# Optimization experiments

Hardware: AMD Instinct MI355X
Metric: run time of the kernel (lower is better)

## Reference

```python
import jax, jax.numpy as jnp
import numpy as np

B, L, D, DEG = 32, 1024, 512, 8
E = B * L * DEG  # 262144 edges total
N = B * L


def setup_inputs() -> dict:
    key = jax.random.key(0)
    ks = jax.random.split(key, 8)
    text_feature = jax.random.normal(ks[0], (B, L, D), jnp.float32)
    # edge list per sample (torch.nonzero(edge_matrix[i]) equivalent), offset by b*L like PyG batching
    src_local = jax.random.randint(ks[1], (E,), 0, L, jnp.int32)
    dst_local = jax.random.randint(ks[2], (E,), 0, L, jnp.int32)
    boff = (jnp.arange(E, dtype=jnp.int32) // (E // B)) * L
    edge_src = src_local + boff
    edge_dst = dst_local + boff
    s = 1.0 / np.sqrt(D)
    W1 = jax.random.uniform(ks[3], (D, D), jnp.float32, -s, s)   # node Linear
    b1 = jax.random.uniform(ks[4], (D,), jnp.float32, -s, s)
    gamma = jnp.ones((D,), jnp.float32)      # BatchNorm1d weight
    beta = jnp.zeros((D,), jnp.float32)      # BatchNorm1d bias
    run_mean = jnp.zeros((D,), jnp.float32)  # BN running stats (eval mode)
    run_var = jnp.ones((D,), jnp.float32)
    alpha1 = jnp.array(0.25, jnp.float32)    # PReLU (node MLP)
    Wg = jax.random.uniform(ks[5], (D, D), jnp.float32, -s, s)   # GCNConv lin (bias=False)
    bg = jnp.zeros((D,), jnp.float32)        # GCNConv bias
    alpha2 = jnp.array(0.25, jnp.float32)    # PReLU (after GCN)
    return {"text_feature": text_feature, "edge_src": edge_src, "edge_dst": edge_dst,
            "W1": W1, "b1": b1, "gamma": gamma, "beta": beta,
            "run_mean": run_mean, "run_var": run_var, "alpha1": alpha1,
            "Wg": Wg, "bg": bg, "alpha2": alpha2}


def reference(text_feature, edge_src, edge_dst, W1, b1, gamma, beta,
              run_mean, run_var, alpha1, Wg, bg, alpha2):
    Bs, Ls, Ds = text_feature.shape
    Nn = Bs * Ls
    xf = text_feature.reshape(Nn, Ds)
    # node MLP: Linear -> BatchNorm1d (eval) -> PReLU
    h = xf @ W1 + b1
    h = (h - run_mean) * jax.lax.rsqrt(run_var + 1e-5) * gamma + beta
    h = jnp.where(h >= 0, h, alpha1 * h)
    # GCNConv: add self loops, symmetric degree norm, gather->scatter-add, + bias
    nodes = jnp.arange(Nn, dtype=edge_src.dtype)
    src = jnp.concatenate([edge_src, nodes])
    dst = jnp.concatenate([edge_dst, nodes])
    deg = jnp.zeros((Nn,), h.dtype).at[dst].add(1.0)  # in-degree incl. self loop, >= 1
    dinv = jax.lax.rsqrt(deg)
    xw = h @ Wg                               # [N, D]
    msg = (xw * dinv[:, None])[src]           # gather D^{-1/2}-scaled messages [E+N, D]
    agg = jnp.zeros_like(xw).at[dst].add(msg) * dinv[:, None]
    g = agg + bg
    g = jnp.where(g >= 0, g, alpha2 * g)      # PReLU
    g = g.reshape(Bs, Ls, Ds)
    # F.normalize(p=2, dim=2) + residual (original input)
    g = g / jnp.clip(jnp.linalg.norm(g, axis=2, keepdims=True), 1e-12)
    return g + text_feature
```

## Files before the change

### kernel.cpp

```cpp
#include <hip/hip_runtime.h>
#include <math.h>

#define DD    512
#define NN    32768
#define EE    262144

typedef float f32x4 __attribute__((ext_vector_type(4)));
typedef __bf16 bf16x8 __attribute__((ext_vector_type(8)));
typedef __bf16 bf16x4 __attribute__((ext_vector_type(4)));

__global__ void k_zero(int* __restrict__ cnt) {
    int i = blockIdx.x * 256 + threadIdx.x;
    if (i < NN) cnt[i] = 0;
}

__global__ void k_count(const int* __restrict__ dst, int* __restrict__ cnt) {
    int e = blockIdx.x * 256 + threadIdx.x;
    if (e < EE) atomicAdd(&cnt[dst[e]], 1);
}

__global__ __launch_bounds__(1024) void k_scan(
    const int* __restrict__ cnt, int* __restrict__ offs,
    int* __restrict__ cursor, float* __restrict__ dinv)
{
    __shared__ int part[1024];
    int t = threadIdx.x;
    int base = t * 32;
    int local[32];
    int s = 0;
#pragma unroll
    for (int i = 0; i < 32; ++i) { local[i] = s; s += cnt[base + i]; }
    part[t] = s;
    __syncthreads();
    for (int off = 1; off < 1024; off <<= 1) {
        int v = (t >= off) ? part[t - off] : 0;
        __syncthreads();
        part[t] += v;
        __syncthreads();
    }
    int prev = (t == 0) ? 0 : part[t - 1];
#pragma unroll
    for (int i = 0; i < 32; ++i) {
        int o = prev + local[i];
        offs[base + i] = o;
        cursor[base + i] = o;
        dinv[base + i] = rsqrtf((float)cnt[base + i] + 1.0f);
    }
    if (t == 1023) offs[NN] = part[1023];
}

__global__ void k_fill(const int* __restrict__ src, const int* __restrict__ dst,
                       int* __restrict__ cursor, int* __restrict__ csr) {
    int e = blockIdx.x * 256 + threadIdx.x;
    if (e < EE) {
        int d = dst[e];
        int p = atomicAdd(&cursor[d], 1);
        csr[p] = src[e];
    }
}

__global__ __launch_bounds__(256) void k_wt(const float* __restrict__ W1, const float* __restrict__ Wg,
                                            __bf16* __restrict__ W1t, __bf16* __restrict__ Wgt) {
    __shared__ float tile[32][33];
    const float* W = blockIdx.z ? Wg : W1;
    __bf16* Wt = blockIdx.z ? Wgt : W1t;
    int x0 = blockIdx.x * 32;
    int y0 = blockIdx.y * 32;
    int tx = threadIdx.x;
    for (int j = threadIdx.y; j < 32; j += 8)
        tile[j][tx] = W[(size_t)(y0 + j) * DD + x0 + tx];
    __syncthreads();
    for (int j = threadIdx.y; j < 32; j += 8)
        Wt[(size_t)(x0 + j) * DD + y0 + tx] = (__bf16)tile[tx][j];
}

template <int MODE>
__global__ __launch_bounds__(256) void k_gemm_mfma(
    const void* __restrict__ Ap,
    const __bf16* __restrict__ Bt,
    __bf16* __restrict__ Cout,
    const float* __restrict__ bias,
    const float* __restrict__ gamma, const float* __restrict__ beta,
    const float* __restrict__ mean, const float* __restrict__ var,
    const float* __restrict__ alphap,
    const float* __restrict__ dinv)
{
    __shared__ __bf16 lds[2][128 * 32];

    const int tid  = threadIdx.x;
    const int lane = tid & 63;
    const int w    = tid >> 6;
    const int wm   = (w >> 1) * 64;
    const int wn   = (w & 1) * 64;
    const int work = ((blockIdx.x & 7) << 7) + (blockIdx.x >> 3);
    const int m0   = (work >> 2) * 128;
    const int n0   = (work & 3) * 128;

    f32x4 acc[4][4] = {};

    for (int k0 = 0; k0 < DD; k0 += 32) {
        __syncthreads();
#pragma unroll
        for (int rd = 0; rd < 2; ++rd) {
            int cbase = rd * 256 + w * 64;
            int cidx = cbase + lane;
            int r = cidx >> 2, s = cidx & 3;
            int c = s ^ ((r >> 1) & 3);
            const __bf16* gb = Bt + (size_t)(n0 + r) * DD + k0 + c * 8;
            __builtin_amdgcn_global_load_lds(
                (const __attribute__((address_space(1))) unsigned int*)gb,
                (__attribute__((address_space(3))) unsigned int*)(&lds[1][cbase * 8]), 16, 0, 0);
        }
        if constexpr (MODE == 1) {
            const float* A = (const float*)Ap;
#pragma unroll
            for (int hh = 0; hh < 2; ++hh) {
                int ci = tid + hh * 256;
                int r = ci >> 2, s = ci & 3;
                int c = s ^ ((r >> 1) & 3);
                const float* ga = A + (size_t)(m0 + r) * DD + k0 + c * 8;
                float4 f0 = *(const float4*)ga;
                float4 f1 = *(const float4*)(ga + 4);
                bf16x8 o;
                o[0] = (__bf16)f0.x; o[1] = (__bf16)f0.y; o[2] = (__bf16)f0.z; o[3] = (__bf16)f0.w;
                o[4] = (__bf16)f1.x; o[5] = (__bf16)f1.y; o[6] = (__bf16)f1.z; o[7] = (__bf16)f1.w;
                *(bf16x8*)&lds[0][ci * 8] = o;
            }
        } else {
            const __bf16* A = (const __bf16*)Ap;
#pragma unroll
            for (int rd = 0; rd < 2; ++rd) {
                int cbase = rd * 256 + w * 64;
                int cidx = cbase + lane;
                int r = cidx >> 2, s = cidx & 3;
                int c = s ^ ((r >> 1) & 3);
                const __bf16* ga = A + (size_t)(m0 + r) * DD + k0 + c * 8;
                __builtin_amdgcn_global_load_lds(
                    (const __attribute__((address_space(1))) unsigned int*)ga,
                    (__attribute__((address_space(3))) unsigned int*)(&lds[0][cbase * 8]), 16, 0, 0);
            }
        }
        __syncthreads();

        bf16x8 af[4], bf[4];
#pragma unroll
        for (int m = 0; m < 4; ++m) {
            int r = wm + m * 16 + (lane & 15);
            int s = (lane >> 4) ^ ((r >> 1) & 3);
            af[m] = *(const bf16x8*)&lds[0][r * 32 + s * 8];
            int q = wn + m * 16 + (lane & 15);
            int sq = (lane >> 4) ^ ((q >> 1) & 3);
            bf[m] = *(const bf16x8*)&lds[1][q * 32 + sq * 8];
        }
#pragma unroll
        for (int m = 0; m < 4; ++m)
#pragma unroll
            for (int n = 0; n < 4; ++n)
                acc[m][n] = __builtin_amdgcn_mfma_f32_16x16x32_bf16(af[m], bf[n], acc[m][n], 0, 0, 0);
    }

    float alpha = (MODE == 1) ? alphap[0] : 0.0f;
#pragma unroll
    for (int m = 0; m < 4; ++m) {
        int row_base = m0 + wm + m * 16 + ((lane >> 4) << 2);
#pragma unroll
        for (int n = 0; n < 4; ++n) {
            int col = n0 + wn + n * 16 + (lane & 15);
#pragma unroll
            for (int j = 0; j < 4; ++j) {
                int row = row_base + j;
                float x = acc[m][n][j];
                if (MODE == 1) {
                    x += bias[col];
                    x = (x - mean[col]) * rsqrtf(var[col] + 1e-5f) * gamma[col] + beta[col];
                    x = (x >= 0.0f) ? x : alpha * x;
                } else {
                    x *= dinv[row];
                }
                Cout[(size_t)row * DD + col] = (__bf16)x;
            }
        }
    }
}

__global__ __launch_bounds__(256) void k_gather_final(
    const int* __restrict__ offs, const int* __restrict__ csr,
    const __bf16* __restrict__ xws, const float* __restrict__ dinv,
    const float* __restrict__ bg, const float* __restrict__ alpha2,
    const float* __restrict__ text, float* __restrict__ out)
{
    int blk = blockIdx.x;
    int sb  = ((blk & 7) << 10) + (blk >> 3);
    int wave = threadIdx.x >> 6;
    int lane = threadIdx.x & 63;
    int node = sb * 4 + wave;
    int c = lane * 8;
    int beg = offs[node], end = offs[node + 1];
    int ne = end - beg;

    bf16x8 sv = *(const bf16x8*)(xws + (size_t)node * DD + c);
    float a[8];
#pragma unroll
    for (int i = 0; i < 8; ++i) a[i] = (float)sv[i];

    int k = 0;
    for (; k + 4 <= ne; k += 4) {
        int s0 = csr[beg + k + 0];
        int s1 = csr[beg + k + 1];
        int s2 = csr[beg + k + 2];
        int s3 = csr[beg + k + 3];
        bf16x8 v0 = *(const bf16x8*)(xws + (size_t)s0 * DD + c);
        bf16x8 v1 = *(const bf16x8*)(xws + (size_t)s1 * DD + c);
        bf16x8 v2 = *(const bf16x8*)(xws + (size_t)s2 * DD + c);
        bf16x8 v3 = *(const bf16x8*)(xws + (size_t)s3 * DD + c);
#pragma unroll
        for (int i = 0; i < 8; ++i)
            a[i] += (float)v0[i] + (float)v1[i] + (float)v2[i] + (float)v3[i];
    }
    for (; k < ne; ++k) {
        int s = csr[beg + k];
        bf16x8 v = *(const bf16x8*)(xws + (size_t)s * DD + c);
#pragma unroll
        for (int i = 0; i < 8; ++i) a[i] += (float)v[i];
    }

    float di = dinv[node];
    float al = alpha2[0];
    float g[8];
    float ss = 0.0f;
#pragma unroll
    for (int i = 0; i < 8; ++i) {
        float x = a[i] * di + bg[c + i];
        x = (x >= 0.0f) ? x : al * x;
        g[i] = x;
        ss += x * x;
    }
#pragma unroll
    for (int off = 1; off < 64; off <<= 1) ss += __shfl_xor(ss, off, 64);
    float inv = 1.0f / fmaxf(sqrtf(ss), 1e-12f);

    float4 t0 = *(const float4*)(text + (size_t)node * DD + c);
    float4 t1 = *(const float4*)(text + (size_t)node * DD + c + 4);
    float4 o0, o1;
    o0.x = g[0] * inv + t0.x; o0.y = g[1] * inv + t0.y;
    o0.z = g[2] * inv + t0.z; o0.w = g[3] * inv + t0.w;
    o1.x = g[4] * inv + t1.x; o1.y = g[5] * inv + t1.y;
    o1.z = g[6] * inv + t1.z; o1.w = g[7] * inv + t1.w;
    *(float4*)(out + (size_t)node * DD + c)     = o0;
    *(float4*)(out + (size_t)node * DD + c + 4) = o1;
}

extern "C" void kernel_launch(void* const* d_in, const int* in_sizes, int n_in,
                              void* d_out, int out_size, void* d_ws, size_t ws_size,
                              hipStream_t stream) {
    const float* text   = (const float*)d_in[0];
    const int*   esrc   = (const int*)d_in[1];
    const int*   edst   = (const int*)d_in[2];
    const float* W1     = (const float*)d_in[3];
    const float* b1     = (const float*)d_in[4];
    const float* gamma  = (const float*)d_in[5];
    const float* beta   = (const float*)d_in[6];
    const float* rmean  = (const float*)d_in[7];
    const float* rvar   = (const float*)d_in[8];
    const float* alpha1 = (const float*)d_in[9];
    const float* Wg     = (const float*)d_in[10];
    const float* bg     = (const float*)d_in[11];
    const float* alpha2 = (const float*)d_in[12];
    float* out = (float*)d_out;

    char* p = (char*)d_ws;
    auto alloc = [&](size_t bytes) { char* r = p; p += (bytes + 255) & ~(size_t)255; return r; };
    int*    cnt     = (int*)alloc((size_t)NN * 4);
    int*    offs    = (int*)alloc((size_t)(NN + 1) * 4);
    int*    cursor  = (int*)alloc((size_t)NN * 4);
    float*  dinv    = (float*)alloc((size_t)NN * 4);
    int*    csr     = (int*)alloc((size_t)EE * 4);
    __bf16* W1t     = (__bf16*)alloc((size_t)DD * DD * 2);
    __bf16* Wgt     = (__bf16*)alloc((size_t)DD * DD * 2);
    __bf16* h_bf    = (__bf16*)alloc((size_t)NN * DD * 2);
    __bf16* xws     = (__bf16*)alloc((size_t)NN * DD * 2);

    k_zero<<<NN / 256, 256, 0, stream>>>(cnt);
    k_count<<<EE / 256, 256, 0, stream>>>(edst, cnt);
    k_scan<<<1, 1024, 0, stream>>>(cnt, offs, cursor, dinv);
    k_fill<<<EE / 256, 256, 0, stream>>>(esrc, edst, cursor, csr);

    k_wt<<<dim3(16, 16, 2), dim3(32, 8), 0, stream>>>(W1, Wg, W1t, Wgt);

    k_gemm_mfma<1><<<1024, 256, 0, stream>>>(text, W1t, h_bf, b1, gamma, beta, rmean, rvar, alpha1, nullptr);

    k_gemm_mfma<2><<<1024, 256, 0, stream>>>(h_bf, Wgt, xws, nullptr, nullptr, nullptr, nullptr, nullptr, nullptr, dinv);

    k_gather_final<<<NN / 4, 256, 0, stream>>>(offs, csr, xws, dinv, bg, alpha2, text, out);
}
```

Before: 154.4 us.

## Double-buffer GEMM LDS tiles to overlap global loads with MFMA compute

Splits the shared-memory tile into separate double-buffered A and B buffers and software-pipelines the K loop. The next K-slice is prefetched (via global_load_lds, or into registers for the fp32 A path) while the current slice feeds the MFMAs. This leaves one barrier per iteration instead of two. It is meant to hide global-load latency behind matrix math, at the cost of doubled LDS use and extra registers, which may lower occupancy.

```diff
diff --git a/kernel.cpp b/kernel.cpp
--- a/kernel.cpp
+++ b/kernel.cpp
@@ -85,7 +85,8 @@
     const float* __restrict__ alphap,
     const float* __restrict__ dinv)
 {
-    __shared__ __bf16 lds[2][128 * 32];
+    __shared__ __bf16 As[2][128 * 32];
+    __shared__ __bf16 Bs[2][128 * 32];
 
     const int tid  = threadIdx.x;
     const int lane = tid & 63;
@@ -97,9 +98,9 @@
     const int n0   = (work & 3) * 128;
 
     f32x4 acc[4][4] = {};
-
-    for (int k0 = 0; k0 < DD; k0 += 32) {
-        __syncthreads();
+    float4 fa[2][2];
+
+    auto stageB = [&](int bb, int k0) {
 #pragma unroll
         for (int rd = 0; rd < 2; ++rd) {
             int cbase = rd * 256 + w * 64;
@@ -109,54 +110,92 @@
             const __bf16* gb = Bt + (size_t)(n0 + r) * DD + k0 + c * 8;
             __builtin_amdgcn_global_load_lds(
                 (const __attribute__((address_space(1))) unsigned int*)gb,
-                (__attribute__((address_space(3))) unsigned int*)(&lds[1][cbase * 8]), 16, 0, 0);
-        }
-        if constexpr (MODE == 1) {
-            const float* A = (const float*)Ap;
-#pragma unroll
-            for (int hh = 0; hh < 2; ++hh) {
-                int ci = tid + hh * 256;
-                int r = ci >> 2, s = ci & 3;
-                int c = s ^ ((r >> 1) & 3);
-                const float* ga = A + (size_t)(m0 + r) * DD + k0 + c * 8;
-                float4 f0 = *(const float4*)ga;
-                float4 f1 = *(const float4*)(ga + 4);
-                bf16x8 o;
-                o[0] = (__bf16)f0.x; o[1] = (__bf16)f0.y; o[2] = (__bf16)f0.z; o[3] = (__bf16)f0.w;
-                o[4] = (__bf16)f1.x; o[5] = (__bf16)f1.y; o[6] = (__bf16)f1.z; o[7] = (__bf16)f1.w;
-                *(bf16x8*)&lds[0][ci * 8] = o;
-            }
-        } else {
-            const __bf16* A = (const __bf16*)Ap;
-#pragma unroll
-            for (int rd = 0; rd < 2; ++rd) {
-                int cbase = rd * 256 + w * 64;
-                int cidx = cbase + lane;
-                int r = cidx >> 2, s = cidx & 3;
-                int c = s ^ ((r >> 1) & 3);
-                const __bf16* ga = A + (size_t)(m0 + r) * DD + k0 + c * 8;
-                __builtin_amdgcn_global_load_lds(
-                    (const __attribute__((address_space(1))) unsigned int*)ga,
-                    (__attribute__((address_space(3))) unsigned int*)(&lds[0][cbase * 8]), 16, 0, 0);
-            }
-        }
-        __syncthreads();
-
-        bf16x8 af[4], bf[4];
+                (__attribute__((address_space(3))) unsigned int*)(&Bs[bb][cbase * 8]), 16, 0, 0);
+        }
+    };
+    auto stageA_lds = [&](int bb, int k0) {
+        const __bf16* A = (const __bf16*)Ap;
+#pragma unroll
+        for (int rd = 0; rd < 2; ++rd) {
+            int cbase = rd * 256 + w * 64;
+            int cidx = cbase + lane;
+            int r = cidx >> 2, s = cidx & 3;
+            int c = s ^ ((r >> 1) & 3);
+            const __bf16* ga = A + (size_t)(m0 + r) * DD + k0 + c * 8;
+            __builtin_amdgcn_global_load_lds(
+                (const __attribute__((address_space(1))) unsigned int*)ga,
+                (__attribute__((address_space(3))) unsigned int*)(&As[bb][cbase * 8]), 16, 0, 0);
+        }
+    };
+    auto loadA = [&](int k0) {
+        const float* A = (const float*)Ap;
+#pragma unroll
+        for (int hh = 0; hh < 2; ++hh) {
+            int ci = tid + hh * 256;
+            int r = ci >> 2, s = ci & 3;
+            int c = s ^ ((r >> 1) & 3);
+            const float* ga = A + (size_t)(m0 + r) * DD + k0 + c * 8;
+            fa[hh][0] = *(const float4*)ga;
+            fa[hh][1] = *(const float4*)(ga + 4);
+        }
+    };
+    auto writeA = [&](int bb) {
+#pragma unroll
+        for (int hh = 0; hh < 2; ++hh) {
+            int ci = tid + hh * 256;
+            bf16x8 o;
+            o[0] = (__bf16)fa[hh][0].x; o[1] = (__bf16)fa[hh][0].y;
+            o[2] = (__bf16)fa[hh][0].z; o[3] = (__bf16)fa[hh][0].w;
+            o[4] = (__bf16)fa[hh][1].x; o[5] = (__bf16)fa[hh][1].y;
+            o[6] = (__bf16)fa[hh][1].z; o[7] = (__bf16)fa[hh][1].w;
+            *(bf16x8*)&As[bb][ci * 8] = o;
+        }
+    };
+
+    if constexpr (MODE == 1) {
+        loadA(0);
+        stageB(0, 0);
+        writeA(0);
+    } else {
+        stageA_lds(0, 0);
+        stageB(0, 0);
+    }
+    __syncthreads();
+
+#pragma unroll
+    for (int kt = 0; kt < 16; ++kt) {
+        const int cur = kt & 1;
+        const int nxt = cur ^ 1;
+        const int k1  = (kt + 1) * 32;
+
+        bf16x8 af[4], bfr[4];
 #pragma unroll
         for (int m = 0; m < 4; ++m) {
             int r = wm + m * 16 + (lane & 15);
             int s = (lane >> 4) ^ ((r >> 1) & 3);
-            af[m] = *(const bf16x8*)&lds[0][r * 32 + s * 8];
+            af[m] = *(const bf16x8*)&As[cur][r * 32 + s * 8];
             int q = wn + m * 16 + (lane & 15);
             int sq = (lane >> 4) ^ ((q >> 1) & 3);
-            bf[m] = *(const bf16x8*)&lds[1][q * 32 + sq * 8];
-        }
+            bfr[m] = *(const bf16x8*)&Bs[cur][q * 32 + sq * 8];
+        }
+
+        if (kt < 15) {
+            if constexpr (MODE == 1) loadA(k1);
+            else                     stageA_lds(nxt, k1);
+            stageB(nxt, k1);
+        }
+
 #pragma unroll
         for (int m = 0; m < 4; ++m)
 #pragma unroll
             for (int n = 0; n < 4; ++n)
-                acc[m][n] = __builtin_amdgcn_mfma_f32_16x16x32_bf16(af[m], bf[n], acc[m][n], 0, 0, 0);
+                acc[m][n] = __builtin_amdgcn_mfma_f32_16x16x32_bf16(af[m], bfr[n], acc[m][n], 0, 0, 0);
+
+        if constexpr (MODE == 1) {
+            if (kt < 15) writeA(nxt);
+        }
+
+        __syncthreads();
     }
 
     float alpha = (MODE == 1) ? alphap[0] : 0.0f;
```

After: 152.2 us. About the same (-1.4%).

## Keep weight slice in registers and stream A row slabs through LDS

Applied to the files above, without the earlier changes.

Replaces the 128x128 LDS-tiled GEMM with a weight-stationary kernel. Each wave holds a 32-column slice of the transposed weight (full K) in registers, and the block streams 32-row slabs of A (full K=512) through double-buffered LDS, so weight tiles are no longer reloaded for every K step. The BatchNorm affine transform is folded into a per-column scale and shift. The per-row dinv scaling moves from the second GEMM epilogue into the gather, which now applies dinv of each source node as it reads it. The change adds heavy register pressure (32 bf16x8 weight fragments per lane), only 256 blocks of 512 threads, small 32x32-per-wave MFMA tiles, and extra scalar dinv loads per edge.

```diff
diff --git a/kernel.cpp b/kernel.cpp
--- a/kernel.cpp
+++ b/kernel.cpp
@@ -7,7 +7,9 @@
 
 typedef float f32x4 __attribute__((ext_vector_type(4)));
 typedef __bf16 bf16x8 __attribute__((ext_vector_type(8)));
-typedef __bf16 bf16x4 __attribute__((ext_vector_type(4)));
+
+#define AS1 __attribute__((address_space(1)))
+#define AS3 __attribute__((address_space(3)))
 
 __global__ void k_zero(int* __restrict__ cnt) {
     int i = blockIdx.x * 256 + threadIdx.x;
@@ -75,111 +77,135 @@
 }
 
 template <int MODE>
-__global__ __launch_bounds__(256) void k_gemm_mfma(
+__global__ __launch_bounds__(512, 2) void k_gemm_w(
     const void* __restrict__ Ap,
-    const __bf16* __restrict__ Bt,
+    const __bf16* __restrict__ Wt,
     __bf16* __restrict__ Cout,
     const float* __restrict__ bias,
     const float* __restrict__ gamma, const float* __restrict__ beta,
     const float* __restrict__ mean, const float* __restrict__ var,
-    const float* __restrict__ alphap,
-    const float* __restrict__ dinv)
+    const float* __restrict__ alphap)
 {
-    __shared__ __bf16 lds[2][128 * 32];
-
-    const int tid  = threadIdx.x;
-    const int lane = tid & 63;
-    const int w    = tid >> 6;
-    const int wm   = (w >> 1) * 64;
-    const int wn   = (w & 1) * 64;
-    const int work = ((blockIdx.x & 7) << 7) + (blockIdx.x >> 3);
-    const int m0   = (work >> 2) * 128;
-    const int n0   = (work & 3) * 128;
-
-    f32x4 acc[4][4] = {};
-
-    for (int k0 = 0; k0 < DD; k0 += 32) {
+    __shared__ __bf16 slab[2][32 * DD];
+
+    const int t    = threadIdx.x;
+    const int lane = t & 63;
+    const int wv   = t >> 6;
+    const int work = ((blockIdx.x & 7) << 5) + (blockIdx.x >> 3);
+    const int nsl  = work & 1;
+    const int mb   = work >> 1;
+    const int mbase   = mb * 256;
+    const int colbase = nsl * 256 + wv * 32;
+
+    bf16x8 wf[2][16];
+#pragma unroll
+    for (int C = 0; C < 2; ++C)
+#pragma unroll
+        for (int kf = 0; kf < 16; ++kf) {
+            int col = colbase + C * 16 + (lane & 15);
+            wf[C][kf] = *(const bf16x8*)(Wt + (size_t)col * DD + kf * 32 + (lane >> 4) * 8);
+        }
+
+    float s0 = 0, s1 = 0, t0 = 0, t1 = 0, al = 0;
+    if constexpr (MODE == 1) {
+        int c0 = colbase + (lane & 15), c1 = c0 + 16;
+        float r0 = rsqrtf(var[c0] + 1e-5f), r1 = rsqrtf(var[c1] + 1e-5f);
+        s0 = gamma[c0] * r0;  s1 = gamma[c1] * r1;
+        t0 = (bias[c0] - mean[c0]) * s0 + beta[c0];
+        t1 = (bias[c1] - mean[c1]) * s1 + beta[c1];
+        al = alphap[0];
+    }
+
+    float4 fa[4][2];
+
+    auto loadA1 = [&](int mt) {
+        const float* A = (const float*)Ap;
+#pragma unroll
+        for (int q = 0; q < 4; ++q) {
+            int ci = q * 512 + t;
+            int r = ci >> 6, c = ci & 63;
+            const float* g = A + (size_t)(mbase + mt * 32 + r) * DD + c * 8;
+            fa[q][0] = *(const float4*)g;
+            fa[q][1] = *(const float4*)(g + 4);
+        }
+    };
+    auto writeA1 = [&](int bb) {
+#pragma unroll
+        for (int q = 0; q < 4; ++q) {
+            int ci = q * 512 + t;
+            int r = ci >> 6, c = ci & 63;
+            bf16x8 o;
+            o[0] = (__bf16)fa[q][0].x; o[1] = (__bf16)fa[q][0].y;
+            o[2] = (__bf16)fa[q][0].z; o[3] = (__bf16)fa[q][0].w;
+            o[4] = (__bf16)fa[q][1].x; o[5] = (__bf16)fa[q][1].y;
+            o[6] = (__bf16)fa[q][1].z; o[7] = (__bf16)fa[q][1].w;
+            *(bf16x8*)&slab[bb][r * DD + (c ^ (r & 7)) * 8] = o;
+        }
+    };
+    auto stage2 = [&](int bb, int mt) {
+        const __bf16* A = (const __bf16*)Ap;
+#pragma unroll
+        for (int q = 0; q < 4; ++q) {
+            int ci = q * 512 + wv * 64 + lane;
+            int r = ci >> 6, c = ci & 63;
+            int cl = c ^ (r & 7);
+            const __bf16* g = A + (size_t)(mbase + mt * 32 + r) * DD + cl * 8;
+            __builtin_amdgcn_global_load_lds(
+                (const AS1 unsigned int*)g,
+                (AS3 unsigned int*)(&slab[bb][(q * 512 + wv * 64) * 8]), 16, 0, 0);
+        }
+    };
+
+    if constexpr (MODE == 1) { loadA1(0); writeA1(0); }
+    else                     { stage2(0, 0); }
+    __syncthreads();
+
+#pragma unroll
+    for (int mt = 0; mt < 8; ++mt) {
+        const int cur = mt & 1, nxt = cur ^ 1;
+
+        if (mt < 7) {
+            if constexpr (MODE == 1) loadA1(mt + 1);
+            else                     stage2(nxt, mt + 1);
+        }
+
+        f32x4 acc[2][2] = {};
+        const __bf16* sl = &slab[cur][0];
+#pragma unroll
+        for (int kf = 0; kf < 16; ++kf) {
+            int r0 = (lane & 15), r1 = 16 + (lane & 15);
+            int c  = kf * 4 + (lane >> 4);
+            bf16x8 a0 = *(const bf16x8*)&sl[r0 * DD + (c ^ (r0 & 7)) * 8];
+            bf16x8 a1 = *(const bf16x8*)&sl[r1 * DD + (c ^ (r1 & 7)) * 8];
+            acc[0][0] = __builtin_amdgcn_mfma_f32_16x16x32_bf16(a0, wf[0][kf], acc[0][0], 0, 0, 0);
+            acc[0][1] = __builtin_amdgcn_mfma_f32_16x16x32_bf16(a0, wf[1][kf], acc[0][1], 0, 0, 0);
+            acc[1][0] = __builtin_amdgcn_mfma_f32_16x16x32_bf16(a1, wf[0][kf], acc[1][0], 0, 0, 0);
+            acc[1][1] = __builtin_amdgcn_mfma_f32_16x16x32_bf16(a1, wf[1][kf], acc[1][1], 0, 0, 0);
+        }
+
+#pragma unroll
+        for (int R = 0; R < 2; ++R)
+#pragma unroll
+            for (int C = 0; C < 2; ++C) {
+                int col  = colbase + C * 16 + (lane & 15);
+                int rowb = mbase + mt * 32 + R * 16 + ((lane >> 4) << 2);
+                float ss = C ? s1 : s0, tt = C ? t1 : t0;
+#pragma unroll
+                for (int j = 0; j < 4; ++j) {
+                    float x = acc[R][C][j];
+                    if constexpr (MODE == 1) {
+                        x = x * ss + tt;
+                        x = (x >= 0.0f) ? x : al * x;
+                    }
+                    Cout[(size_t)(rowb + j) * DD + col] = (__bf16)x;
+                }
+            }
+
+        if constexpr (MODE == 1) {
+            if (mt < 7) writeA1(nxt);
+        }
+
         __syncthreads();
-#pragma unroll
-        for (int rd = 0; rd < 2; ++rd) {
-            int cbase = rd * 256 + w * 64;
-            int cidx = cbase + lane;
-            int r = cidx >> 2, s = cidx & 3;
-            int c = s ^ ((r >> 1) & 3);
-            const __bf16* gb = Bt + (size_t)(n0 + r) * DD + k0 + c * 8;
-            __builtin_amdgcn_global_load_lds(
-                (const __attribute__((address_space(1))) unsigned int*)gb,
-                (__attribute__((address_space(3))) unsigned int*)(&lds[1][cbase * 8]), 16, 0, 0);
-        }
-        if constexpr (MODE == 1) {
-            const float* A = (const float*)Ap;
-#pragma unroll
-            for (int hh = 0; hh < 2; ++hh) {
-                int ci = tid + hh * 256;
-                int r = ci >> 2, s = ci & 3;
-                int c = s ^ ((r >> 1) & 3);
-                const float* ga = A + (size_t)(m0 + r) * DD + k0 + c * 8;
-                float4 f0 = *(const float4*)ga;
-                float4 f1 = *(const float4*)(ga + 4);
-                bf16x8 o;
-                o[0] = (__bf16)f0.x; o[1] = (__bf16)f0.y; o[2] = (__bf16)f0.z; o[3] = (__bf16)f0.w;
-                o[4] = (__bf16)f1.x; o[5] = (__bf16)f1.y; o[6] = (__bf16)f1.z; o[7] = (__bf16)f1.w;
-                *(bf16x8*)&lds[0][ci * 8] = o;
-            }
-        } else {
-            const __bf16* A = (const __bf16*)Ap;
-#pragma unroll
-            for (int rd = 0; rd < 2; ++rd) {
-                int cbase = rd * 256 + w * 64;
-                int cidx = cbase + lane;
-                int r = cidx >> 2, s = cidx & 3;
-                int c = s ^ ((r >> 1) & 3);
-                const __bf16* ga = A + (size_t)(m0 + r) * DD + k0 + c * 8;
-                __builtin_amdgcn_global_load_lds(
-                    (const __attribute__((address_space(1))) unsigned int*)ga,
-                    (__attribute__((address_space(3))) unsigned int*)(&lds[0][cbase * 8]), 16, 0, 0);
-            }
-        }
-        __syncthreads();
-
-        bf16x8 af[4], bf[4];
-#pragma unroll
-        for (int m = 0; m < 4; ++m) {
-            int r = wm + m * 16 + (lane & 15);
-            int s = (lane >> 4) ^ ((r >> 1) & 3);
-            af[m] = *(const bf16x8*)&lds[0][r * 32 + s * 8];
-            int q = wn + m * 16 + (lane & 15);
-            int sq = (lane >> 4) ^ ((q >> 1) & 3);
-            bf[m] = *(const bf16x8*)&lds[1][q * 32 + sq * 8];
-        }
-#pragma unroll
-        for (int m = 0; m < 4; ++m)
-#pragma unroll
-            for (int n = 0; n < 4; ++n)
-                acc[m][n] = __builtin_amdgcn_mfma_f32_16x16x32_bf16(af[m], bf[n], acc[m][n], 0, 0, 0);
-    }
-
-    float alpha = (MODE == 1) ? alphap[0] : 0.0f;
-#pragma unroll
-    for (int m = 0; m < 4; ++m) {
-        int row_base = m0 + wm + m * 16 + ((lane >> 4) << 2);
-#pragma unroll
-        for (int n = 0; n < 4; ++n) {
-            int col = n0 + wn + n * 16 + (lane & 15);
-#pragma unroll
-            for (int j = 0; j < 4; ++j) {
-                int row = row_base + j;
-                float x = acc[m][n][j];
-                if (MODE == 1) {
-                    x += bias[col];
-                    x = (x - mean[col]) * rsqrtf(var[col] + 1e-5f) * gamma[col] + beta[col];
-                    x = (x >= 0.0f) ? x : alpha * x;
-                } else {
-                    x *= dinv[row];
-                }
-                Cout[(size_t)row * DD + col] = (__bf16)x;
-            }
-        }
     }
 }
 
@@ -198,10 +224,11 @@
     int beg = offs[node], end = offs[node + 1];
     int ne = end - beg;
 
+    float dn = dinv[node];
     bf16x8 sv = *(const bf16x8*)(xws + (size_t)node * DD + c);
     float a[8];
 #pragma unroll
-    for (int i = 0; i < 8; ++i) a[i] = (float)sv[i];
+    for (int i = 0; i < 8; ++i) a[i] = dn * (float)sv[i];
 
     int k = 0;
     for (; k + 4 <= ne; k += 4) {
@@ -209,28 +236,29 @@
         int s1 = csr[beg + k + 1];
         int s2 = csr[beg + k + 2];
         int s3 = csr[beg + k + 3];
+        float d0 = dinv[s0], d1 = dinv[s1], d2 = dinv[s2], d3 = dinv[s3];
         bf16x8 v0 = *(const bf16x8*)(xws + (size_t)s0 * DD + c);
         bf16x8 v1 = *(const bf16x8*)(xws + (size_t)s1 * DD + c);
         bf16x8 v2 = *(const bf16x8*)(xws + (size_t)s2 * DD + c);
         bf16x8 v3 = *(const bf16x8*)(xws + (size_t)s3 * DD + c);
 #pragma unroll
         for (int i = 0; i < 8; ++i)
-            a[i] += (float)v0[i] + (float)v1[i] + (float)v2[i] + (float)v3[i];
+            a[i] += d0 * (float)v0[i] + d1 * (float)v1[i] + d2 * (float)v2[i] + d3 * (float)v3[i];
     }
     for (; k < ne; ++k) {
         int s = csr[beg + k];
+        float ds_ = dinv[s];
         bf16x8 v = *(const bf16x8*)(xws + (size_t)s * DD + c);
 #pragma unroll
-        for (int i = 0; i < 8; ++i) a[i] += (float)v[i];
-    }
-
-    float di = dinv[node];
+        for (int i = 0; i < 8; ++i) a[i] += ds_ * (float)v[i];
+    }
+
     float al = alpha2[0];
     float g[8];
     float ss = 0.0f;
 #pragma unroll
     for (int i = 0; i < 8; ++i) {
-        float x = a[i] * di + bg[c + i];
+        float x = a[i] * dn + bg[c + i];
         x = (x >= 0.0f) ? x : al * x;
         g[i] = x;
         ss += x * x;
@@ -287,9 +315,9 @@
 
     k_wt<<<dim3(16, 16, 2), dim3(32, 8), 0, stream>>>(W1, Wg, W1t, Wgt);
 
-    k_gemm_mfma<1><<<1024, 256, 0, stream>>>(text, W1t, h_bf, b1, gamma, beta, rmean, rvar, alpha1, nullptr);
-
-    k_gemm_mfma<2><<<1024, 256, 0, stream>>>(h_bf, Wgt, xws, nullptr, nullptr, nullptr, nullptr, nullptr, nullptr, dinv);
+    k_gemm_w<1><<<256, 512, 0, stream>>>(text, W1t, h_bf, b1, gamma, beta, rmean, rvar, alpha1);
+
+    k_gemm_w<2><<<256, 512, 0, stream>>>(h_bf, Wgt, xws, nullptr, nullptr, nullptr, nullptr, nullptr, nullptr);
 
     k_gather_final<<<NN / 4, 256, 0, stream>>>(offs, csr, xws, dinv, bg, alpha2, text, out);
 }
```

Result: faster. 142.6 us (-7.6%).
